# Kernel optimization log

Hardware: AMD Instinct MI355X
Metric: run time of the kernel (lower is better)

The kernel has to match this reference:

```python
import jax, jax.numpy as jnp
import numpy as np

EMBED_DIM = 1024
NUM_HEADS = 16
HEAD_DIM = EMBED_DIM // NUM_HEADS
WINDOW = 256


def setup_inputs() -> dict:
    key = jax.random.key(0)
    ks = jax.random.split(key, 9)
    B, S, E = 4, 4096, EMBED_DIM
    sc = 1.0 / np.sqrt(E)
    return {
        "x": jax.random.normal(ks[0], (B, S, E), jnp.float32),
        "Wq": jax.random.normal(ks[1], (E, E), jnp.float32) * sc,
        "bq": jax.random.normal(ks[2], (E,), jnp.float32) * 0.01,
        "Wk": jax.random.normal(ks[3], (E, E), jnp.float32) * sc,
        "bk": jax.random.normal(ks[4], (E,), jnp.float32) * 0.01,
        "Wv": jax.random.normal(ks[5], (E, E), jnp.float32) * sc,
        "bv": jax.random.normal(ks[6], (E,), jnp.float32) * 0.01,
        "Wo": jax.random.normal(ks[7], (E, E), jnp.float32) * sc,
        "bo": jax.random.normal(ks[8], (E,), jnp.float32) * 0.01,
    }


def reference(x, Wq, bq, Wk, bk, Wv, bv, Wo, bo):
    B, S, E = x.shape
    H, D, W = NUM_HEADS, HEAD_DIM, WINDOW
    NW = S // W  # seq_len chosen divisible by window -> no padding

    def split_heads(t):  # [B,S,E] -> [B,H,NW,W,D]
        return t.reshape(B, S, H, D).transpose(0, 2, 1, 3).reshape(B, H, NW, W, D)

    q = split_heads(x @ Wq + bq)
    k = split_heads(x @ Wk + bk)
    v = split_heads(x @ Wv + bv)

    # block-diagonal attention within each non-overlapping window
    scores = jnp.einsum("bhnqd,bhnkd->bhnqk", q, k) / jnp.sqrt(
        jnp.asarray(D, x.dtype))
    attn = jax.nn.softmax(scores, axis=-1)
    out = jnp.einsum("bhnqk,bhnkd->bhnqd", attn, v)  # [B,H,NW,W,D]

    out = out.reshape(B, H, S, D).transpose(0, 2, 1, 3).reshape(B, S, E)
    return out @ Wo + bo
```

## Files before the change

### kernel.cpp

```cpp
#include <hip/hip_runtime.h>

typedef __bf16 bf16x8 __attribute__((ext_vector_type(8)));
typedef float  f32x4  __attribute__((ext_vector_type(4)));

#define MFMA(a,b,c) __builtin_amdgcn_mfma_f32_16x16x32_bf16((a),(b),(c),0,0,0)

__device__ __forceinline__ unsigned short f2bf(float f){
  unsigned u = __builtin_bit_cast(unsigned, f);
  u += 0x7fffu + ((u>>16)&1u);
  return (unsigned short)(u>>16);
}
__device__ __forceinline__ unsigned pack_bf2(float a, float b){
  return (unsigned)f2bf(a) | ((unsigned)f2bf(b)<<16);
}
__device__ __forceinline__ void gload_lds16(const void* g, void* l){
  __builtin_amdgcn_global_load_lds((__attribute__((address_space(1))) void*)(g),
                                   (__attribute__((address_space(3))) void*)(l), 16, 0, 0);
}

__global__ void k_cvt_x(const float* __restrict__ x, unsigned short* __restrict__ o){
  const size_t t = (size_t)blockIdx.x*256 + threadIdx.x;
  #pragma unroll
  for (int i=0;i<4;i++){
    size_t idx = t + (size_t)i*1048576;
    float4 f = ((const float4*)x)[idx];
    ((uint2*)o)[idx] = make_uint2(pack_bf2(f.x,f.y), pack_bf2(f.z,f.w));
  }
}

__global__ void k_cvt_wT(const float* __restrict__ Wq, const float* __restrict__ Wk,
                         const float* __restrict__ Wv, const float* __restrict__ Wo,
                         unsigned short* __restrict__ wT){
  const int z = blockIdx.z;
  const float* W = (z==0)?Wq:(z==1)?Wk:(z==2)?Wv:Wo;
  unsigned short* out = wT + (size_t)z*1048576;
  __shared__ float tile[32][33];
  const int r0 = blockIdx.y*32, c0 = blockIdx.x*32;
  const int r = threadIdx.x>>5, c = threadIdx.x&31;
  #pragma unroll
  for (int i=0;i<4;i++) tile[r + i*8][c] = W[(size_t)(r0 + r + i*8)*1024 + c0 + c];
  __syncthreads();
  #pragma unroll
  for (int i=0;i<4;i++)
    out[(size_t)(c0 + r + i*8)*1024 + r0 + c] = f2bf(tile[c][r + i*8]);
}

#define QUAD(MF0, KS) do { \
  _Pragma("unroll") \
  for (int mf_=0; mf_<4; ++mf_){ \
    _Pragma("unroll") \
    for (int nf_=0; nf_<4; ++nf_) \
      acc[MF0+mf_][nf_] = MFMA(aF[KS][MF0+mf_], bF[KS][nf_], acc[MF0+mf_][nf_]); \
  } } while(0)

template<int MODE>
__global__ __launch_bounds__(512,2) void k_gemm8(const unsigned short* __restrict__ A,
                       const unsigned short* __restrict__ Bm,
                       const float* __restrict__ bias0, const float* __restrict__ bias1,
                       const float* __restrict__ bias2,
                       unsigned short* __restrict__ q_ws, unsigned short* __restrict__ k_ws,
                       unsigned short* __restrict__ v_ws, float* __restrict__ outf)
{
  __shared__ char smem[131072];
  const int tid = threadIdx.x, lane = tid&63, wid = tid>>6;
  const int g = lane>>4, l15 = lane&15;
  const int wr = wid>>2, wc = wid&3;

  constexpr int NBX = (MODE==0)? 12 : 4;
  constexpr int CPX = (MODE==0)? 96 : 32;
  const int flat = blockIdx.y*NBX + blockIdx.x;
  const int swz  = (flat&7)*CPX + (flat>>3);
  const int m0 = (swz/NBX)<<8, n0 = (swz%NBX)<<8;

  auto stage = [&](int h){
    const int t = h>>2, kind = h&3, hf = kind&1;
    char* ldst = smem + ((kind<2)?0:65536) + (t&1)*32768 + hf*16384 + wid*1024;
    const unsigned short* gbase = (kind<2)? A : Bm;
    const int row0 = ((kind<2)? m0 : n0) + hf*128;
    #pragma unroll
    for (int j=0;j<2;j++){
      const int o = (j*512 + tid)*16;
      const int r = o>>7, cb = o&127;
      const int cs = cb ^ ((r&7)<<4);
      gload_lds16((const char*)gbase + (size_t)(row0 + r)*2048 + t*128 + cs,
                  ldst + j*8192);
    }
  };

  f32x4 acc[8][4];
  #pragma unroll
  for (int i=0;i<8;i++)
    #pragma unroll
    for (int j=0;j<4;j++) acc[i][j] = f32x4{0.f,0.f,0.f,0.f};

  #pragma unroll
  for (int h=0;h<6;++h) stage(h);
  asm volatile("s_waitcnt vmcnt(4)" ::: "memory");
  __builtin_amdgcn_s_barrier();
  __builtin_amdgcn_sched_barrier(0);

  for (int t=0;t<16;++t){
    const char* Ab = smem + (t&1)*32768 + wr*16384;
    const char* Bb = smem + 65536 + (t&1)*32768 + (wc>>1)*16384;
    const int brow = (wc&1)*64;
    const int sw = (l15&7)<<4;
    bf16x8 aF[2][8], bF[2][4];

    #pragma unroll
    for (int mf=0;mf<4;mf++){
      aF[0][mf] = *(const bf16x8*)(Ab + (mf*16+l15)*128 + ((g*16)    ^ sw));
      aF[1][mf] = *(const bf16x8*)(Ab + (mf*16+l15)*128 + ((64+g*16) ^ sw));
    }
    #pragma unroll
    for (int nf=0;nf<4;nf++){
      bF[0][nf] = *(const bf16x8*)(Bb + (brow+nf*16+l15)*128 + ((g*16)    ^ sw));
      bF[1][nf] = *(const bf16x8*)(Bb + (brow+nf*16+l15)*128 + ((64+g*16) ^ sw));
    }
    if (4*t+6 < 64) stage(4*t+6);
    __builtin_amdgcn_sched_barrier(0);
    __builtin_amdgcn_s_barrier();
    __builtin_amdgcn_sched_barrier(0);
    __builtin_amdgcn_s_setprio(1);
    QUAD(0,0);
    __builtin_amdgcn_s_setprio(0);
    __builtin_amdgcn_sched_barrier(0);
    asm volatile("s_waitcnt lgkmcnt(0)" ::: "memory");
    __builtin_amdgcn_s_barrier();
    __builtin_amdgcn_sched_barrier(0);

    #pragma unroll
    for (int mf=4;mf<8;mf++){
      aF[0][mf] = *(const bf16x8*)(Ab + (mf*16+l15)*128 + ((g*16)    ^ sw));
      aF[1][mf] = *(const bf16x8*)(Ab + (mf*16+l15)*128 + ((64+g*16) ^ sw));
    }
    if (4*t+7 < 64) stage(4*t+7);
    __builtin_amdgcn_sched_barrier(0);
    __builtin_amdgcn_s_barrier();
    __builtin_amdgcn_sched_barrier(0);
    __builtin_amdgcn_s_setprio(1);
    QUAD(0,1);
    __builtin_amdgcn_s_setprio(0);
    __builtin_amdgcn_sched_barrier(0);
    asm volatile("s_waitcnt lgkmcnt(0)" ::: "memory");
    __builtin_amdgcn_s_barrier();
    __builtin_amdgcn_sched_barrier(0);

    if (4*t+8 < 64) stage(4*t+8);
    __builtin_amdgcn_sched_barrier(0);
    __builtin_amdgcn_s_barrier();
    __builtin_amdgcn_sched_barrier(0);
    __builtin_amdgcn_s_setprio(1);
    QUAD(4,0);
    __builtin_amdgcn_s_setprio(0);
    __builtin_amdgcn_sched_barrier(0);
    __builtin_amdgcn_s_barrier();
    __builtin_amdgcn_sched_barrier(0);

    if (4*t+9 < 64) stage(4*t+9);
    __builtin_amdgcn_sched_barrier(0);
    __builtin_amdgcn_s_barrier();
    __builtin_amdgcn_sched_barrier(0);
    __builtin_amdgcn_s_setprio(1);
    QUAD(4,1);
    __builtin_amdgcn_s_setprio(0);
    __builtin_amdgcn_sched_barrier(0);
    if (t < 14)       asm volatile("s_waitcnt vmcnt(4)" ::: "memory");
    else if (t == 14) asm volatile("s_waitcnt vmcnt(0)" ::: "memory");
    __builtin_amdgcn_s_barrier();
    __builtin_amdgcn_sched_barrier(0);
  }

  if constexpr (MODE==0){
    const int z  = n0>>10;
    const int nE = n0 & 1023;
    const float* bias = (z==0)? bias0 : (z==1)? bias1 : bias2;
    #pragma unroll
    for (int nf=0;nf<4;nf++){
      const int ncol = nE + wc*64 + nf*16 + l15;
      const float bn = bias[ncol];
      const int h = ncol>>6, d = ncol&63;
      #pragma unroll
      for (int mf=0;mf<8;mf++){
        const int mb = m0 + wr*128 + mf*16 + g*4;
        if (z==2){
          const int b = mb>>12, s = mb&4095, nw = s>>8, w0 = s&255;
          unsigned short pk0=f2bf(acc[mf][nf][0]+bn), pk1=f2bf(acc[mf][nf][1]+bn),
                         pk2=f2bf(acc[mf][nf][2]+bn), pk3=f2bf(acc[mf][nf][3]+bn);
          size_t idx = ((((size_t)(b*16+h)*16 + nw)*64 + d)<<8) + w0;
          *(ushort4*)(v_ws + idx) = make_ushort4(pk0,pk1,pk2,pk3);
        } else {
          unsigned short* dst = (z==0)? q_ws : k_ws;
          const float scale = (z==0)? 0.125f : 1.0f;
          #pragma unroll
          for (int r=0;r<4;r++){
            const int m = mb + r, b = m>>12, s = m&4095;
            dst[(((size_t)(b*16+h)*4096 + s)<<6) + d] = f2bf((acc[mf][nf][r]+bn)*scale);
          }
        }
      }
    }
  } else {
    #pragma unroll
    for (int nf=0;nf<4;nf++){
      const int n = n0 + wc*64 + nf*16 + l15;
      const float bn = bias0[n];
      #pragma unroll
      for (int mf=0;mf<8;mf++)
        #pragma unroll
        for (int r=0;r<4;r++){
          const int m = m0 + wr*128 + mf*16 + g*4 + r;
          outf[(size_t)m*1024 + n] = acc[mf][nf][r] + bn;
        }
    }
  }
}

__global__ __launch_bounds__(256,2) void k_attn(const unsigned short* __restrict__ qw,
                                                const unsigned short* __restrict__ kw,
                                                const unsigned short* __restrict__ vw,
                                                unsigned short* __restrict__ ow)
{
  __shared__ unsigned short Ks[2][4096];
  __shared__ unsigned short Vs[2][4096];
  __shared__ unsigned short Ps[4][4096];
  const int tid = threadIdx.x, lane = tid&63, wid = tid>>6;
  const int g = lane>>4, l15 = lane&15;
  const int bhn = blockIdx.x;
  const int nw = bhn&15, h = (bhn>>4)&15, b = bhn>>8;

  const size_t qkbase = ((size_t)((b*16+h)*4096 + nw*256))<<6;
  const unsigned short* Qg = qw + qkbase;
  const unsigned short* Kg = kw + qkbase;
  const unsigned short* Vg = vw + (((size_t)(b*16+h)*16 + nw)<<14);
  const float NEG_INF = -__builtin_inff();

  bf16x8 qa[4][2];
  #pragma unroll
  for (int qf=0;qf<4;qf++)
    #pragma unroll
    for (int ks=0;ks<2;ks++)
      qa[qf][ks] = *(const bf16x8*)((const char*)Qg + (wid*64 + qf*16 + l15)*128 + ks*64 + g*16);

  auto stage = [&](int kt, int bi){
    #pragma unroll
    for (int i=0;i<4;i++){
      const int chunk = wid*4 + i;
      const int obase = (chunk&7)<<10;
      const int o = obase + lane*16;
      const int r = o>>7, cb = o&127;
      const int cs = cb ^ ((r&7)<<4);
      if (chunk < 8)
        gload_lds16((const char*)Kg + (kt*64 + r)*128 + cs, (char*)Ks[bi] + obase);
      else
        gload_lds16((const char*)Vg + r*512 + kt*128 + cs, (char*)Vs[bi] + obase);
    }
  };

  f32x4 oacc[4][4];
  float mrow[4][4], lrow[4][4];
  #pragma unroll
  for (int i=0;i<4;i++)
    #pragma unroll
    for (int j=0;j<4;j++){ oacc[i][j] = f32x4{0.f,0.f,0.f,0.f}; mrow[i][j] = NEG_INF; lrow[i][j] = 0.f; }

  stage(0,0);
  __syncthreads();
  for (int kt=0;kt<4;kt++){
    const int cur = kt&1;
    if (kt<3) stage(kt+1, cur^1);

    bf16x8 kb[4][2];
    #pragma unroll
    for (int kf=0;kf<4;kf++)
      #pragma unroll
      for (int ks=0;ks<2;ks++){
        const int kr = kf*16 + l15, cb = ks*64 + g*16;
        kb[kf][ks] = *(const bf16x8*)((const char*)Ks[cur] + kr*128 + (cb ^ ((kr&7)<<4)));
      }

    unsigned short* P = Ps[wid];
    #pragma unroll
    for (int qf=0;qf<4;qf++){
      f32x4 sfr[4];
      #pragma unroll
      for (int kf=0;kf<4;kf++){
        f32x4 zz = f32x4{0.f,0.f,0.f,0.f};
        zz = MFMA(qa[qf][0], kb[kf][0], zz);
        sfr[kf] = MFMA(qa[qf][1], kb[kf][1], zz);
      }
      #pragma unroll
      for (int r=0;r<4;r++){
        float t = fmaxf(fmaxf(sfr[0][r],sfr[1][r]), fmaxf(sfr[2][r],sfr[3][r]));
        t = fmaxf(t, __shfl_xor(t,1,64)); t = fmaxf(t, __shfl_xor(t,2,64));
        t = fmaxf(t, __shfl_xor(t,4,64)); t = fmaxf(t, __shfl_xor(t,8,64));
        const float mo = mrow[qf][r];
        const float mn = fmaxf(mo, t);
        const float alpha = __expf(mo - mn);
        float rs = 0.f;
        #pragma unroll
        for (int kf=0;kf<4;kf++){ float p = __expf(sfr[kf][r]-mn); sfr[kf][r] = p; rs += p; }
        rs += __shfl_xor(rs,1,64); rs += __shfl_xor(rs,2,64);
        rs += __shfl_xor(rs,4,64); rs += __shfl_xor(rs,8,64);
        lrow[qf][r] = lrow[qf][r]*alpha + rs;
        mrow[qf][r] = mn;
        #pragma unroll
        for (int df=0;df<4;df++) oacc[qf][df][r] *= alpha;
        const int prow = qf*16 + g*4 + r;
        const int sw = (prow&7)<<4;
        char* Pb = (char*)P + prow*128;
        #pragma unroll
        for (int kf=0;kf<4;kf++)
          *(unsigned short*)(Pb + (((kf*16 + l15)*2) ^ sw)) = f2bf(sfr[kf][r]);
      }
    }
    __builtin_amdgcn_sched_barrier(0);

    bf16x8 vb[4][2];
    #pragma unroll
    for (int df=0;df<4;df++)
      #pragma unroll
      for (int ks=0;ks<2;ks++){
        const int d = df*16 + l15, cb = ks*64 + g*16;
        vb[df][ks] = *(const bf16x8*)((const char*)Vs[cur] + d*128 + (cb ^ ((d&7)<<4)));
      }
    #pragma unroll
    for (int qf=0;qf<4;qf++){
      const int pr = qf*16 + l15;
      const bf16x8 pa0 = *(const bf16x8*)((const char*)P + pr*128 + ((g*16)      ^ ((pr&7)<<4)));
      const bf16x8 pa1 = *(const bf16x8*)((const char*)P + pr*128 + ((64 + g*16) ^ ((pr&7)<<4)));
      #pragma unroll
      for (int df=0;df<4;df++){
        oacc[qf][df] = MFMA(pa0, vb[df][0], oacc[qf][df]);
        oacc[qf][df] = MFMA(pa1, vb[df][1], oacc[qf][df]);
      }
    }
    __syncthreads();
  }

  #pragma unroll
  for (int qf=0;qf<4;qf++)
    #pragma unroll
    for (int r=0;r<4;r++){
      const float inv = 1.f / lrow[qf][r];
      const int srow = nw*256 + wid*64 + qf*16 + g*4 + r;
      const size_t base = ((size_t)b*4096 + srow)*1024 + (size_t)h*64;
      #pragma unroll
      for (int df=0;df<4;df++)
        ow[base + df*16 + l15] = f2bf(oacc[qf][df][r]*inv);
    }
}

extern "C" void kernel_launch(void* const* d_in, const int* in_sizes, int n_in,
                              void* d_out, int out_size, void* d_ws, size_t ws_size,
                              hipStream_t stream)
{
  const float* x  = (const float*)d_in[0];
  const float* Wq = (const float*)d_in[1];
  const float* bq = (const float*)d_in[2];
  const float* Wk = (const float*)d_in[3];
  const float* bk = (const float*)d_in[4];
  const float* Wv = (const float*)d_in[5];
  const float* bv = (const float*)d_in[6];
  const float* Wo = (const float*)d_in[7];
  const float* bo = (const float*)d_in[8];
  float* out = (float*)d_out;

  char* ws = (char*)d_ws;
  unsigned short* xbf  = (unsigned short*)(ws);
  unsigned short* wT   = (unsigned short*)(ws + (size_t)32*1048576);
  unsigned short* q_ws = (unsigned short*)(ws + (size_t)40*1048576);
  unsigned short* k_ws = (unsigned short*)(ws + (size_t)72*1048576);
  unsigned short* v_ws = (unsigned short*)(ws + (size_t)104*1048576);
  unsigned short* obf  = xbf;

  k_cvt_x<<<4096,256,0,stream>>>(x, xbf);
  k_cvt_wT<<<dim3(32,32,4),256,0,stream>>>(Wq,Wk,Wv,Wo, wT);
  k_gemm8<0><<<dim3(12,64),512,0,stream>>>(xbf, wT, bq,bk,bv, q_ws,k_ws,v_ws, nullptr);
  k_attn<<<1024,256,0,stream>>>(q_ws,k_ws,v_ws, obf);
  k_gemm8<1><<<dim3(4,64),512,0,stream>>>(obf, wT + (size_t)3*1048576, bo,nullptr,nullptr,
                                          nullptr,nullptr,nullptr, out);
}
```

Baseline: 261.4 us.

## Reorder GEMM prefetch schedule and split fragment loads by K-half

Restructures the bf16 GEMM main loop. A fragments and B fragments are now loaded per K-half into smaller register arrays (aK0/aK1/bK0/bK1) instead of one large aF/bF set. The global-to-LDS staging is reordered so A is prefetched one tile ahead and B two tiles ahead. B's next-next tile is written into the current buffer only after all B reads for the current tile have finished. The goal is lower register pressure and more MFMA/load overlap per phase, at the cost of extra LDS reads for A and tighter barrier ordering.

```diff
diff --git a/kernel.cpp b/kernel.cpp
--- a/kernel.cpp
+++ b/kernel.cpp
@@ -4,6 +4,7 @@
 typedef float  f32x4  __attribute__((ext_vector_type(4)));
 
 #define MFMA(a,b,c) __builtin_amdgcn_mfma_f32_16x16x32_bf16((a),(b),(c),0,0,0)
+#define SB() __builtin_amdgcn_sched_barrier(0)
 
 __device__ __forceinline__ unsigned short f2bf(float f){
   unsigned u = __builtin_bit_cast(unsigned, f);
@@ -45,12 +46,12 @@
     out[(size_t)(c0 + r + i*8)*1024 + r0 + c] = f2bf(tile[c][r + i*8]);
 }
 
-#define QUAD(MF0, KS) do { \
+#define QUAD16(AF, BF, MF0) do { \
   _Pragma("unroll") \
   for (int mf_=0; mf_<4; ++mf_){ \
     _Pragma("unroll") \
     for (int nf_=0; nf_<4; ++nf_) \
-      acc[MF0+mf_][nf_] = MFMA(aF[KS][MF0+mf_], bF[KS][nf_], acc[MF0+mf_][nf_]); \
+      acc[MF0+mf_][nf_] = MFMA(AF[mf_], BF[nf_], acc[MF0+mf_][nf_]); \
   } } while(0)
 
 template<int MODE>
@@ -72,17 +73,16 @@
   const int swz  = (flat&7)*CPX + (flat>>3);
   const int m0 = (swz/NBX)<<8, n0 = (swz%NBX)<<8;
 
-  auto stage = [&](int h){
-    const int t = h>>2, kind = h&3, hf = kind&1;
-    char* ldst = smem + ((kind<2)?0:65536) + (t&1)*32768 + hf*16384 + wid*1024;
-    const unsigned short* gbase = (kind<2)? A : Bm;
-    const int row0 = ((kind<2)? m0 : n0) + hf*128;
+  auto stageH = [&](int isA, int tt, int hf){
+    char* ldst = smem + (isA?0:65536) + (tt&1)*32768 + hf*16384 + wid*1024;
+    const unsigned short* gbase = isA? A : Bm;
+    const int row0 = (isA? m0 : n0) + hf*128;
     #pragma unroll
     for (int j=0;j<2;j++){
       const int o = (j*512 + tid)*16;
       const int r = o>>7, cb = o&127;
       const int cs = cb ^ ((r&7)<<4);
-      gload_lds16((const char*)gbase + (size_t)(row0 + r)*2048 + t*128 + cs,
+      gload_lds16((const char*)gbase + (size_t)(row0 + r)*2048 + (tt<<7) + cs,
                   ldst + j*8192);
     }
   };
@@ -93,81 +93,85 @@
     #pragma unroll
     for (int j=0;j<4;j++) acc[i][j] = f32x4{0.f,0.f,0.f,0.f};
 
-  #pragma unroll
-  for (int h=0;h<6;++h) stage(h);
+  stageH(1,0,0); stageH(1,0,1);
+  stageH(0,0,0); stageH(0,0,1);
+  stageH(1,1,0); stageH(1,1,1);
   asm volatile("s_waitcnt vmcnt(4)" ::: "memory");
   __builtin_amdgcn_s_barrier();
-  __builtin_amdgcn_sched_barrier(0);
-
+  SB();
+
+  const int sw = (l15&7)<<4;
   for (int t=0;t<16;++t){
     const char* Ab = smem + (t&1)*32768 + wr*16384;
     const char* Bb = smem + 65536 + (t&1)*32768 + (wc>>1)*16384;
     const int brow = (wc&1)*64;
-    const int sw = (l15&7)<<4;
-    bf16x8 aF[2][8], bF[2][4];
-
-    #pragma unroll
-    for (int mf=0;mf<4;mf++){
-      aF[0][mf] = *(const bf16x8*)(Ab + (mf*16+l15)*128 + ((g*16)    ^ sw));
-      aF[1][mf] = *(const bf16x8*)(Ab + (mf*16+l15)*128 + ((64+g*16) ^ sw));
-    }
-    #pragma unroll
-    for (int nf=0;nf<4;nf++){
-      bF[0][nf] = *(const bf16x8*)(Bb + (brow+nf*16+l15)*128 + ((g*16)    ^ sw));
-      bF[1][nf] = *(const bf16x8*)(Bb + (brow+nf*16+l15)*128 + ((64+g*16) ^ sw));
-    }
-    if (4*t+6 < 64) stage(4*t+6);
-    __builtin_amdgcn_sched_barrier(0);
-    __builtin_amdgcn_s_barrier();
-    __builtin_amdgcn_sched_barrier(0);
+    bf16x8 aK0[4], aK1[4], bK0[4], bK1[4];
+
+    #pragma unroll
+    for (int mf=0;mf<4;mf++)
+      aK0[mf] = *(const bf16x8*)(Ab + (mf*16+l15)*128 + ((g*16) ^ sw));
+    #pragma unroll
+    for (int nf=0;nf<4;nf++)
+      bK0[nf] = *(const bf16x8*)(Bb + (brow+nf*16+l15)*128 + ((g*16) ^ sw));
+    if (t+1 < 16) stageH(0, t+1, 0);
+    SB();
+    __builtin_amdgcn_s_barrier();
+    asm volatile("s_waitcnt lgkmcnt(0)" ::: "memory");
+    SB();
     __builtin_amdgcn_s_setprio(1);
-    QUAD(0,0);
+    QUAD16(aK0, bK0, 0);
     __builtin_amdgcn_s_setprio(0);
-    __builtin_amdgcn_sched_barrier(0);
+    SB();
+    __builtin_amdgcn_s_barrier();
+    SB();
+
+    #pragma unroll
+    for (int mf=0;mf<4;mf++)
+      aK1[mf] = *(const bf16x8*)(Ab + (mf*16+l15)*128 + ((64+g*16) ^ sw));
+    #pragma unroll
+    for (int nf=0;nf<4;nf++)
+      bK1[nf] = *(const bf16x8*)(Bb + (brow+nf*16+l15)*128 + ((64+g*16) ^ sw));
+    if (t+1 < 16) stageH(0, t+1, 1);
+    SB();
+    __builtin_amdgcn_s_barrier();
     asm volatile("s_waitcnt lgkmcnt(0)" ::: "memory");
-    __builtin_amdgcn_s_barrier();
-    __builtin_amdgcn_sched_barrier(0);
-
-    #pragma unroll
-    for (int mf=4;mf<8;mf++){
-      aF[0][mf] = *(const bf16x8*)(Ab + (mf*16+l15)*128 + ((g*16)    ^ sw));
-      aF[1][mf] = *(const bf16x8*)(Ab + (mf*16+l15)*128 + ((64+g*16) ^ sw));
-    }
-    if (4*t+7 < 64) stage(4*t+7);
-    __builtin_amdgcn_sched_barrier(0);
-    __builtin_amdgcn_s_barrier();
-    __builtin_amdgcn_sched_barrier(0);
+    SB();
     __builtin_amdgcn_s_setprio(1);
-    QUAD(0,1);
+    QUAD16(aK1, bK1, 0);
     __builtin_amdgcn_s_setprio(0);
-    __builtin_amdgcn_sched_barrier(0);
+    SB();
+    __builtin_amdgcn_s_barrier();
+    SB();
+
+    #pragma unroll
+    for (int mf=0;mf<4;mf++)
+      aK0[mf] = *(const bf16x8*)(Ab + ((4+mf)*16+l15)*128 + ((g*16) ^ sw));
+    #pragma unroll
+    for (int mf=0;mf<4;mf++)
+      aK1[mf] = *(const bf16x8*)(Ab + ((4+mf)*16+l15)*128 + ((64+g*16) ^ sw));
+    SB();
+    __builtin_amdgcn_s_barrier();
     asm volatile("s_waitcnt lgkmcnt(0)" ::: "memory");
-    __builtin_amdgcn_s_barrier();
-    __builtin_amdgcn_sched_barrier(0);
-
-    if (4*t+8 < 64) stage(4*t+8);
-    __builtin_amdgcn_sched_barrier(0);
-    __builtin_amdgcn_s_barrier();
-    __builtin_amdgcn_sched_barrier(0);
+    SB();
     __builtin_amdgcn_s_setprio(1);
-    QUAD(4,0);
+    QUAD16(aK0, bK0, 4);
     __builtin_amdgcn_s_setprio(0);
-    __builtin_amdgcn_sched_barrier(0);
-    __builtin_amdgcn_s_barrier();
-    __builtin_amdgcn_sched_barrier(0);
-
-    if (4*t+9 < 64) stage(4*t+9);
-    __builtin_amdgcn_sched_barrier(0);
-    __builtin_amdgcn_s_barrier();
-    __builtin_amdgcn_sched_barrier(0);
+    SB();
+    __builtin_amdgcn_s_barrier();
+    SB();
+
+    if (t+2 < 16){ stageH(1, t+2, 0); stageH(1, t+2, 1); }
+    SB();
+    __builtin_amdgcn_s_barrier();
+    SB();
     __builtin_amdgcn_s_setprio(1);
-    QUAD(4,1);
+    QUAD16(aK1, bK1, 4);
     __builtin_amdgcn_s_setprio(0);
-    __builtin_amdgcn_sched_barrier(0);
+    SB();
     if (t < 14)       asm volatile("s_waitcnt vmcnt(4)" ::: "memory");
     else if (t == 14) asm volatile("s_waitcnt vmcnt(0)" ::: "memory");
     __builtin_amdgcn_s_barrier();
-    __builtin_amdgcn_sched_barrier(0);
+    SB();
   }
 
   if constexpr (MODE==0){
```

Result: no change. 260.0 us (-0.5%).
